# Kernel optimization log

Hardware: AMD Instinct MI355X
Metric: run time of the kernel (lower is better)

## Reference

```python
import jax, jax.numpy as jnp
import numpy as np

EPS = 1e-09

def setup_inputs() -> dict:
    key = jax.random.key(0)
    k1, k2, k3 = jax.random.split(key, 3)
    B, C, H, W = 16, 512, 64, 64
    K = 64  # node_num
    x = jax.random.normal(k1, (B, C, H, W), dtype=jnp.float32)
    anchor = jax.random.uniform(k2, (K, C), dtype=jnp.float32)
    sigma_raw = jax.random.uniform(k3, (K, C), dtype=jnp.float32)
    return {"x": x, "anchor": anchor, "sigma_raw": sigma_raw}

def _l2norm(v, axis):
    return v / jnp.maximum(jnp.linalg.norm(v, axis=axis, keepdims=True), 1e-12)

def reference(x, anchor, sigma_raw):
    B, C, H, W = x.shape
    K = anchor.shape[0]
    N = H * W
    sigma = jax.nn.sigmoid(sigma_raw)               # [K, C]
    xf = x.reshape(B, C, N).transpose(0, 2, 1)      # [B, N, C] descriptors

    # squared Mahalanobis-like distance ||(x - a_k)/s_k||^2 via expansion
    # (avoids materializing the [B, N, K, C] residual the torch loop builds)
    inv_s2 = 1.0 / (sigma * sigma)                  # [K, C]
    a_s2 = anchor * inv_s2                          # [K, C]
    const = jnp.sum(anchor * a_s2, axis=1)          # [K]
    d2 = (jnp.einsum('bnc,kc->bnk', xf * xf, inv_s2)
          - 2.0 * jnp.einsum('bnc,kc->bnk', xf, a_s2)
          + const[None, None, :])                   # [B, N, K]
    logits = (-0.5 * d2).transpose(0, 2, 1)         # [B, K, N]
    soft_assign = jax.nn.softmax(logits, axis=1)    # softmax over nodes

    # aggregation: nodes[b,k,c] = sum_n w * (x - a_k)/s_k / (sum_n w + eps)
    w_sum = jnp.sum(soft_assign, axis=2)            # [B, K]
    wx = jnp.einsum('bkn,bnc->bkc', soft_assign, xf)  # [B, K, C]
    nodes = (wx - w_sum[:, :, None] * anchor[None]) / sigma[None]
    nodes = nodes / (w_sum[:, :, None] + EPS)       # [B, K, C]

    nodes = _l2norm(nodes, axis=2)                  # intra-normalize per node
    flat = _l2norm(nodes.reshape(B, -1), axis=1)    # global L2
    # faithful to torch: flat [B, K*C] reinterpreted (no transpose) as [B, C, K]
    return flat.reshape(B, C, K), soft_assign
```

## Files before the change

### kernel.cpp

```cpp
#include <hip/hip_runtime.h>
#include <math.h>

#define B_ 16
#define C_ 512
#define N_ 4096
#define K_ 64

#define OFF_PBIG    0
#define OFF_INVSIG  131072
#define OFF_WSUM    163840
#define OFF_GSUM    164864
#define OFF_WX      164992

typedef short bf16x8 __attribute__((ext_vector_type(8)));
typedef float f32x16 __attribute__((ext_vector_type(16)));

union U4 { uint4 u; bf16x8 b; };

__device__ __forceinline__ unsigned hi16(float f) { return __float_as_uint(f) >> 16; }
__device__ __forceinline__ unsigned hi16rne(float f) {
  return (__float_as_uint(f) + 0x8000u) >> 16;
}
__device__ __forceinline__ float fromhi(unsigned h) { return __uint_as_float(h << 16); }
__device__ __forceinline__ unsigned pk(float lo, float hi) {
  return (__float_as_uint(lo) >> 16) | (__float_as_uint(hi) & 0xFFFF0000u);
}

__global__ void k_prep(const float* __restrict__ anchor,
                       const float* __restrict__ sraw,
                       unsigned* __restrict__ pbig,
                       float* __restrict__ invsig,
                       float* __restrict__ wsum,
                       float* __restrict__ gsum) {
  const int k = blockIdx.x;
  const int t = threadIdx.x;
  __shared__ float s_is2[C_], s_m[C_];
  __shared__ float red[4];
  float part = 0.f;
#pragma unroll
  for (int r = 0; r < 2; r++) {
    int c = r * 256 + t;
    float a = anchor[k * C_ + c];
    float sg = 1.f / (1.f + __expf(-sraw[k * C_ + c]));
    float is = 1.f / sg;
    float is2 = is * is;
    s_is2[c] = is2;
    s_m[c] = -2.f * a * is2;
    invsig[k * C_ + c] = is;
    part = fmaf(a * a, is2, part);
  }
  float v = part;
#pragma unroll
  for (int off = 32; off; off >>= 1) v += __shfl_down(v, off);
  if ((t & 63) == 0) red[t >> 6] = v;
  __syncthreads();
  float cst = red[0] + red[1] + red[2] + red[3];
  unsigned ch = hi16(cst);
  unsigned clr = hi16rne(cst - fromhi(ch));
#pragma unroll
  for (int r = 0; r < 2; r++) {
    int c = r * 256 + t;
    float is2 = s_is2[c], m = s_m[c];
    unsigned ih = hi16(is2);
    unsigned ilr = hi16rne(is2 - fromhi(ih));
    unsigned mh = hi16(m);
    unsigned mlr = hi16rne(m - fromhi(mh));
    unsigned* p = pbig + (size_t)k * 2048 + c * 4;
    p[0] = ih | (ilr << 16);
    p[1] = ih | (mh << 16);
    p[2] = mlr | (mh << 16);
    p[3] = (c == 0) ? (ch | (clr << 16)) : 0u;
  }
  if (k == 0) {
    for (int i = t; i < B_ * K_; i += 256) wsum[i] = 0.f;
    if (t < B_) gsum[t] = 0.f;
  }
}

__global__ __launch_bounds__(256) void k_dist(
    const float* __restrict__ x,
    const unsigned* __restrict__ pbig,
    float* __restrict__ soft,
    float* __restrict__ wsum) {
  const int b = blockIdx.y;
  const int nblk = blockIdx.x * 256;
  const int tid = threadIdx.x;
  const int wid = tid >> 6;
  const int lane = tid & 63;
  const int l31 = lane & 31;
  const int lh = lane >> 5;
  const int n0 = nblk + wid * 64;

  __shared__ unsigned ldsA[64 * 132];

  f32x16 acc[2][2];
#pragma unroll
  for (int kt = 0; kt < 2; kt++)
#pragma unroll
    for (int ns = 0; ns < 2; ns++)
#pragma unroll
      for (int i = 0; i < 16; i++) acc[kt][ns][i] = 0.f;

  const float* xb = x + (size_t)b * (C_ * N_);

  for (int chunk = 0; chunk < 16; chunk++) {
    const uint4* src = (const uint4*)pbig;
#pragma unroll
    for (int it = 0; it < 8; it++) {
      int flat = tid + it * 256;
      int k = flat >> 5, q = flat & 31;
      uint4 vv = src[(size_t)k * 512 + chunk * 32 + q];
      *(uint4*)&ldsA[k * 132 + q * 4] = vv;
    }
    __syncthreads();
    const int cchunk = chunk * 32;
    for (int kstep = 0; kstep < 16; kstep++) {
      U4 a0, a1;
      a0.u = *(const uint4*)&ldsA[l31 * 132 + kstep * 8 + lh * 4];
      a1.u = *(const uint4*)&ldsA[(32 + l31) * 132 + kstep * 8 + lh * 4];
      const int c = cchunk + kstep * 2 + lh;
      const float* xr = xb + (size_t)c * N_;
#pragma unroll
      for (int ns = 0; ns < 2; ns++) {
        float xv = xr[n0 + ns * 32 + l31];
        float x2 = xv * xv;
        unsigned u = __float_as_uint(xv);
        unsigned u2 = __float_as_uint(x2);
        unsigned uhf = u & 0xFFFF0000u;
        unsigned u2hf = u2 & 0xFFFF0000u;
        float xl = xv - __uint_as_float(uhf);
        float x2l = x2 - __uint_as_float(u2hf);
        U4 bf;
        bf.u.x = (u2 >> 16) | u2hf;
        bf.u.y = ((__float_as_uint(x2l) + 0x8000u) >> 16) | uhf;
        bf.u.z = (u >> 16) | ((__float_as_uint(xl) + 0x8000u) & 0xFFFF0000u);
        bf.u.w = (c == 0) ? 0x3F803F80u : 0u;
        acc[0][ns] = __builtin_amdgcn_mfma_f32_32x32x16_bf16(a0.b, bf.b, acc[0][ns], 0, 0, 0);
        acc[1][ns] = __builtin_amdgcn_mfma_f32_32x32x16_bf16(a1.b, bf.b, acc[1][ns], 0, 0, 0);
      }
    }
    __syncthreads();
  }

  float* softb = soft + (size_t)b * (K_ * N_);
#pragma unroll
  for (int ns = 0; ns < 2; ns++) {
    float mm = -3.4e38f;
#pragma unroll
    for (int kt = 0; kt < 2; kt++)
#pragma unroll
      for (int r = 0; r < 16; r++) {
        float l = -0.5f * acc[kt][ns][r];
        acc[kt][ns][r] = l;
        mm = fmaxf(mm, l);
      }
    mm = fmaxf(mm, __shfl_xor(mm, 32));
    float ss = 0.f;
#pragma unroll
    for (int kt = 0; kt < 2; kt++)
#pragma unroll
      for (int r = 0; r < 16; r++) {
        float e = __expf(acc[kt][ns][r] - mm);
        acc[kt][ns][r] = e;
        ss += e;
      }
    ss += __shfl_xor(ss, 32);
    float inv = 1.f / ss;
    const int nc = n0 + ns * 32 + l31;
#pragma unroll
    for (int kt = 0; kt < 2; kt++)
#pragma unroll
      for (int r = 0; r < 16; r++) {
        float w = acc[kt][ns][r] * inv;
        acc[kt][ns][r] = w;
        int k = kt * 32 + (r & 3) + 8 * (r >> 2) + 4 * lh;
        softb[(size_t)k * N_ + nc] = w;
      }
  }
#pragma unroll
  for (int kt = 0; kt < 2; kt++)
#pragma unroll
    for (int r = 0; r < 16; r++) {
      float v = acc[kt][0][r] + acc[kt][1][r];
      v += __shfl_xor(v, 1);
      v += __shfl_xor(v, 2);
      v += __shfl_xor(v, 4);
      v += __shfl_xor(v, 8);
      v += __shfl_xor(v, 16);
      if (l31 == 0) {
        int k = kt * 32 + (r & 3) + 8 * (r >> 2) + 4 * lh;
        atomicAdd(&wsum[b * K_ + k], v);
      }
    }
}

__global__ __launch_bounds__(256) void k_agg(const float* __restrict__ x,
                                             const float* __restrict__ soft,
                                             float* __restrict__ wx) {
  const int ct = blockIdx.x;
  const int b = blockIdx.y;
  const int tid = threadIdx.x;
  const int wid = tid >> 6, lane = tid & 63, l31 = lane & 31, lh = lane >> 5;
  const int c0 = ct * 32;
  const int n0 = wid * 1024;
  __shared__ float red[4][64][36];

  f32x16 acc[2];
#pragma unroll
  for (int kt = 0; kt < 2; kt++)
#pragma unroll
    for (int i = 0; i < 16; i++) acc[kt][i] = 0.f;

  const float* sb = soft + (size_t)b * (K_ * N_);
  const float* xr = x + (size_t)b * (C_ * N_) + (size_t)(c0 + l31) * N_;
  const float* s0 = sb + (size_t)l31 * N_;
  const float* s1 = sb + (size_t)(32 + l31) * N_;

  for (int kstep = 0; kstep < 64; kstep++) {
    int nb = n0 + kstep * 16 + lh * 8;
    float4 f0 = *(const float4*)&s0[nb];
    float4 f1 = *(const float4*)&s0[nb + 4];
    float4 g0 = *(const float4*)&s1[nb];
    float4 g1 = *(const float4*)&s1[nb + 4];
    float4 h0 = *(const float4*)&xr[nb];
    float4 h1 = *(const float4*)&xr[nb + 4];
    U4 A0, A1, Bf;
    A0.u.x = pk(f0.x, f0.y); A0.u.y = pk(f0.z, f0.w);
    A0.u.z = pk(f1.x, f1.y); A0.u.w = pk(f1.z, f1.w);
    A1.u.x = pk(g0.x, g0.y); A1.u.y = pk(g0.z, g0.w);
    A1.u.z = pk(g1.x, g1.y); A1.u.w = pk(g1.z, g1.w);
    Bf.u.x = pk(h0.x, h0.y); Bf.u.y = pk(h0.z, h0.w);
    Bf.u.z = pk(h1.x, h1.y); Bf.u.w = pk(h1.z, h1.w);
    acc[0] = __builtin_amdgcn_mfma_f32_32x32x16_bf16(A0.b, Bf.b, acc[0], 0, 0, 0);
    acc[1] = __builtin_amdgcn_mfma_f32_32x32x16_bf16(A1.b, Bf.b, acc[1], 0, 0, 0);
  }
#pragma unroll
  for (int kt = 0; kt < 2; kt++)
#pragma unroll
    for (int q = 0; q < 4; q++) {
      float4 vv = make_float4(acc[kt][q * 4], acc[kt][q * 4 + 1],
                              acc[kt][q * 4 + 2], acc[kt][q * 4 + 3]);
      *(float4*)&red[wid][lane][kt * 16 + q * 4] = vv;
    }
  __syncthreads();
  const int lt = tid & 63, sb4 = (tid >> 6) * 8;
  float v[8];
#pragma unroll
  for (int i = 0; i < 8; i++) v[i] = 0.f;
#pragma unroll
  for (int w = 0; w < 4; w++)
#pragma unroll
    for (int i = 0; i < 8; i++) v[i] += red[w][lt][sb4 + i];
#pragma unroll
  for (int i = 0; i < 8; i++) {
    int s = sb4 + i;
    int kt = s >> 4, r = s & 15;
    int k = kt * 32 + (r & 3) + 8 * (r >> 2) + 4 * (lt >> 5);
    wx[((size_t)b * K_ + k) * C_ + c0 + (lt & 31)] = v[i];
  }
}

__global__ void k_nodes(const float* __restrict__ wx,
                        const float* __restrict__ wsum,
                        const float* __restrict__ anchor,
                        const float* __restrict__ invsig,
                        float* __restrict__ out0,
                        float* __restrict__ gsum) {
  const int k = blockIdx.x, b = blockIdx.y;
  const int tid = threadIdx.x;
  float wsv = wsum[b * K_ + k];
  float winv = 1.f / (wsv + 1e-9f);
  float vals[4];
  float local = 0.f;
#pragma unroll
  for (int r = 0; r < 4; r++) {
    int c = r * 128 + tid;
    float w = wx[((size_t)b * K_ + k) * C_ + c];
    float v = (w - wsv * anchor[k * C_ + c]) * invsig[k * C_ + c] * winv;
    vals[r] = v;
    local = fmaf(v, v, local);
  }
  float v = local;
#pragma unroll
  for (int off = 32; off; off >>= 1) v += __shfl_down(v, off);
  __shared__ float red[2];
  if ((tid & 63) == 0) red[tid >> 6] = v;
  __syncthreads();
  float sumsq = red[0] + red[1];
  float norm = sqrtf(sumsq);
  float scale = 1.f / fmaxf(norm, 1e-12f);
#pragma unroll
  for (int r = 0; r < 4; r++) {
    int c = r * 128 + tid;
    out0[((size_t)b * K_ + k) * C_ + c] = vals[r] * scale;
  }
  if (tid == 0) atomicAdd(&gsum[b], sumsq * scale * scale);
}

__global__ void k_final(float* __restrict__ out0,
                        const float* __restrict__ gsum) {
  for (int i = blockIdx.x * 256 + threadIdx.x; i < B_ * K_ * C_;
       i += gridDim.x * 256) {
    int b = i >> 15;
    out0[i] = out0[i] * (1.f / fmaxf(sqrtf(gsum[b]), 1e-12f));
  }
}

extern "C" void kernel_launch(void* const* d_in, const int* in_sizes, int n_in,
                              void* d_out, int out_size, void* d_ws, size_t ws_size,
                              hipStream_t stream) {
  const float* x = (const float*)d_in[0];
  const float* anchor = (const float*)d_in[1];
  const float* sraw = (const float*)d_in[2];
  float* out0 = (float*)d_out;
  float* soft = out0 + (size_t)B_ * C_ * K_;
  float* ws = (float*)d_ws;

  unsigned* pbig = (unsigned*)(ws + OFF_PBIG);
  float* invsig = ws + OFF_INVSIG;
  float* wsum = ws + OFF_WSUM;
  float* gsum = ws + OFF_GSUM;
  float* wx = ws + OFF_WX;

  k_prep<<<K_, 256, 0, stream>>>(anchor, sraw, pbig, invsig, wsum, gsum);
  k_dist<<<dim3(N_ / 256, B_), 256, 0, stream>>>(x, pbig, soft, wsum);
  k_agg<<<dim3(C_ / 32, B_), 256, 0, stream>>>(x, soft, wx);
  k_nodes<<<dim3(K_, B_), 128, 0, stream>>>(wx, wsum, anchor, invsig, out0,
                                            gsum);
  k_final<<<512, 256, 0, stream>>>(out0, gsum);
}
```

Before: 305.6 us.

## Prefetch operands, split aggregation over N with LDS tiling, hoist per-node constant

The distance kernel now stages the next chunk's parameters and x values in registers while the current chunk runs on MFMA. Each wave handles 32 positions instead of 64 and the grid is doubled. The per-node constant is added after the matmul instead of being folded into a bf16 slot. The aggregation kernel is restructured to split N into four partitions, tile soft-assign and x through LDS with register prefetch, and write partial sums that the node kernel adds up. Rounding of the low bf16 halves changes from round-to-nearest to truncation, which slightly alters accuracy, and the partial-sum buffer adds extra workspace traffic.

```diff
diff --git a/kernel.cpp b/kernel.cpp
--- a/kernel.cpp
+++ b/kernel.cpp
@@ -7,10 +7,11 @@
 #define K_ 64
 
 #define OFF_PBIG    0
-#define OFF_INVSIG  131072
-#define OFF_WSUM    163840
-#define OFF_GSUM    164864
-#define OFF_WX      164992
+#define OFF_CONST   131072
+#define OFF_INVSIG  131136
+#define OFF_WSUM    163904
+#define OFF_GSUM    164928
+#define OFF_WXP     165120
 
 typedef short bf16x8 __attribute__((ext_vector_type(8)));
 typedef float f32x16 __attribute__((ext_vector_type(16)));
@@ -18,9 +19,6 @@
 union U4 { uint4 u; bf16x8 b; };
 
 __device__ __forceinline__ unsigned hi16(float f) { return __float_as_uint(f) >> 16; }
-__device__ __forceinline__ unsigned hi16rne(float f) {
-  return (__float_as_uint(f) + 0x8000u) >> 16;
-}
 __device__ __forceinline__ float fromhi(unsigned h) { return __uint_as_float(h << 16); }
 __device__ __forceinline__ unsigned pk(float lo, float hi) {
   return (__float_as_uint(lo) >> 16) | (__float_as_uint(hi) & 0xFFFF0000u);
@@ -29,6 +27,7 @@
 __global__ void k_prep(const float* __restrict__ anchor,
                        const float* __restrict__ sraw,
                        unsigned* __restrict__ pbig,
+                       float* __restrict__ constk,
                        float* __restrict__ invsig,
                        float* __restrict__ wsum,
                        float* __restrict__ gsum) {
@@ -54,22 +53,20 @@
   for (int off = 32; off; off >>= 1) v += __shfl_down(v, off);
   if ((t & 63) == 0) red[t >> 6] = v;
   __syncthreads();
-  float cst = red[0] + red[1] + red[2] + red[3];
-  unsigned ch = hi16(cst);
-  unsigned clr = hi16rne(cst - fromhi(ch));
+  if (t == 0) constk[k] = red[0] + red[1] + red[2] + red[3];
 #pragma unroll
   for (int r = 0; r < 2; r++) {
     int c = r * 256 + t;
     float is2 = s_is2[c], m = s_m[c];
     unsigned ih = hi16(is2);
-    unsigned ilr = hi16rne(is2 - fromhi(ih));
+    unsigned il = hi16(is2 - fromhi(ih));
     unsigned mh = hi16(m);
-    unsigned mlr = hi16rne(m - fromhi(mh));
+    unsigned ml = hi16(m - fromhi(mh));
     unsigned* p = pbig + (size_t)k * 2048 + c * 4;
-    p[0] = ih | (ilr << 16);
+    p[0] = ih | (il << 16);
     p[1] = ih | (mh << 16);
-    p[2] = mlr | (mh << 16);
-    p[3] = (c == 0) ? (ch | (clr << 16)) : 0u;
+    p[2] = ml | (mh << 16);
+    p[3] = 0u;
   }
   if (k == 0) {
     for (int i = t; i < B_ * K_; i += 256) wsum[i] = 0.f;
@@ -80,108 +77,118 @@
 __global__ __launch_bounds__(256) void k_dist(
     const float* __restrict__ x,
     const unsigned* __restrict__ pbig,
+    const float* __restrict__ constk,
     float* __restrict__ soft,
     float* __restrict__ wsum) {
   const int b = blockIdx.y;
-  const int nblk = blockIdx.x * 256;
   const int tid = threadIdx.x;
-  const int wid = tid >> 6;
-  const int lane = tid & 63;
-  const int l31 = lane & 31;
-  const int lh = lane >> 5;
-  const int n0 = nblk + wid * 64;
-
+  const int wid = tid >> 6, lane = tid & 63, l31 = lane & 31, lh = lane >> 5;
+  const int n0 = blockIdx.x * 128 + wid * 32;
   __shared__ unsigned ldsA[64 * 132];
-
-  f32x16 acc[2][2];
-#pragma unroll
-  for (int kt = 0; kt < 2; kt++)
-#pragma unroll
-    for (int ns = 0; ns < 2; ns++)
-#pragma unroll
-      for (int i = 0; i < 16; i++) acc[kt][ns][i] = 0.f;
+  __shared__ float csh[64];
+  if (tid < 64) csh[tid] = constk[tid];
+
+  f32x16 acc[2];
+#pragma unroll
+  for (int kt = 0; kt < 2; kt++)
+#pragma unroll
+    for (int i = 0; i < 16; i++) acc[kt][i] = 0.f;
 
   const float* xb = x + (size_t)b * (C_ * N_);
+  const uint4* src = (const uint4*)pbig;
+
+  uint4 preg[8];
+#pragma unroll
+  for (int it = 0; it < 8; it++) {
+    int flat = tid + it * 256;
+    preg[it] = src[(size_t)(flat >> 5) * 512 + (flat & 31)];
+  }
+  float xcur[16], xnext[16];
+#pragma unroll
+  for (int i = 0; i < 16; i++)
+    xcur[i] = xb[(size_t)(i * 2 + lh) * N_ + n0 + l31];
 
   for (int chunk = 0; chunk < 16; chunk++) {
-    const uint4* src = (const uint4*)pbig;
 #pragma unroll
     for (int it = 0; it < 8; it++) {
       int flat = tid + it * 256;
-      int k = flat >> 5, q = flat & 31;
-      uint4 vv = src[(size_t)k * 512 + chunk * 32 + q];
-      *(uint4*)&ldsA[k * 132 + q * 4] = vv;
+      *(uint4*)&ldsA[(flat >> 5) * 132 + (flat & 31) * 4] = preg[it];
     }
     __syncthreads();
-    const int cchunk = chunk * 32;
+    if (chunk < 15) {
+#pragma unroll
+      for (int it = 0; it < 8; it++) {
+        int flat = tid + it * 256;
+        preg[it] = src[(size_t)(flat >> 5) * 512 + (chunk + 1) * 32 + (flat & 31)];
+      }
+#pragma unroll
+      for (int i = 0; i < 16; i++)
+        xnext[i] = xb[(size_t)((chunk + 1) * 32 + i * 2 + lh) * N_ + n0 + l31];
+    }
+#pragma unroll
     for (int kstep = 0; kstep < 16; kstep++) {
       U4 a0, a1;
       a0.u = *(const uint4*)&ldsA[l31 * 132 + kstep * 8 + lh * 4];
       a1.u = *(const uint4*)&ldsA[(32 + l31) * 132 + kstep * 8 + lh * 4];
-      const int c = cchunk + kstep * 2 + lh;
-      const float* xr = xb + (size_t)c * N_;
-#pragma unroll
-      for (int ns = 0; ns < 2; ns++) {
-        float xv = xr[n0 + ns * 32 + l31];
-        float x2 = xv * xv;
-        unsigned u = __float_as_uint(xv);
-        unsigned u2 = __float_as_uint(x2);
-        unsigned uhf = u & 0xFFFF0000u;
-        unsigned u2hf = u2 & 0xFFFF0000u;
-        float xl = xv - __uint_as_float(uhf);
-        float x2l = x2 - __uint_as_float(u2hf);
-        U4 bf;
-        bf.u.x = (u2 >> 16) | u2hf;
-        bf.u.y = ((__float_as_uint(x2l) + 0x8000u) >> 16) | uhf;
-        bf.u.z = (u >> 16) | ((__float_as_uint(xl) + 0x8000u) & 0xFFFF0000u);
-        bf.u.w = (c == 0) ? 0x3F803F80u : 0u;
-        acc[0][ns] = __builtin_amdgcn_mfma_f32_32x32x16_bf16(a0.b, bf.b, acc[0][ns], 0, 0, 0);
-        acc[1][ns] = __builtin_amdgcn_mfma_f32_32x32x16_bf16(a1.b, bf.b, acc[1][ns], 0, 0, 0);
-      }
+      float xv = xcur[kstep];
+      float x2 = xv * xv;
+      unsigned u = __float_as_uint(xv);
+      unsigned u2 = __float_as_uint(x2);
+      unsigned uhf = u & 0xFFFF0000u;
+      unsigned u2hf = u2 & 0xFFFF0000u;
+      float xl = xv - __uint_as_float(uhf);
+      float x2l = x2 - __uint_as_float(u2hf);
+      U4 bf;
+      bf.u.x = (u2 >> 16) | u2hf;
+      bf.u.y = (__float_as_uint(x2l) >> 16) | uhf;
+      bf.u.z = (u >> 16) | (__float_as_uint(xl) & 0xFFFF0000u);
+      bf.u.w = 0u;
+      acc[0] = __builtin_amdgcn_mfma_f32_32x32x16_bf16(a0.b, bf.b, acc[0], 0, 0, 0);
+      acc[1] = __builtin_amdgcn_mfma_f32_32x32x16_bf16(a1.b, bf.b, acc[1], 0, 0, 0);
     }
     __syncthreads();
-  }
+#pragma unroll
+    for (int i = 0; i < 16; i++) xcur[i] = xnext[i];
+  }
+
+  float mm = -3.4e38f;
+#pragma unroll
+  for (int kt = 0; kt < 2; kt++)
+#pragma unroll
+    for (int r = 0; r < 16; r++) {
+      int k = kt * 32 + (r & 3) + 8 * (r >> 2) + 4 * lh;
+      float l = -0.5f * (acc[kt][r] + csh[k]);
+      acc[kt][r] = l;
+      mm = fmaxf(mm, l);
+    }
+  mm = fmaxf(mm, __shfl_xor(mm, 32));
+  float ss = 0.f;
+#pragma unroll
+  for (int kt = 0; kt < 2; kt++)
+#pragma unroll
+    for (int r = 0; r < 16; r++) {
+      float e = __expf(acc[kt][r] - mm);
+      acc[kt][r] = e;
+      ss += e;
+    }
+  ss += __shfl_xor(ss, 32);
+  float inv = 1.f / ss;
 
   float* softb = soft + (size_t)b * (K_ * N_);
 #pragma unroll
-  for (int ns = 0; ns < 2; ns++) {
-    float mm = -3.4e38f;
-#pragma unroll
-    for (int kt = 0; kt < 2; kt++)
-#pragma unroll
-      for (int r = 0; r < 16; r++) {
-        float l = -0.5f * acc[kt][ns][r];
-        acc[kt][ns][r] = l;
-        mm = fmaxf(mm, l);
-      }
-    mm = fmaxf(mm, __shfl_xor(mm, 32));
-    float ss = 0.f;
-#pragma unroll
-    for (int kt = 0; kt < 2; kt++)
-#pragma unroll
-      for (int r = 0; r < 16; r++) {
-        float e = __expf(acc[kt][ns][r] - mm);
-        acc[kt][ns][r] = e;
-        ss += e;
-      }
-    ss += __shfl_xor(ss, 32);
-    float inv = 1.f / ss;
-    const int nc = n0 + ns * 32 + l31;
-#pragma unroll
-    for (int kt = 0; kt < 2; kt++)
-#pragma unroll
-      for (int r = 0; r < 16; r++) {
-        float w = acc[kt][ns][r] * inv;
-        acc[kt][ns][r] = w;
-        int k = kt * 32 + (r & 3) + 8 * (r >> 2) + 4 * lh;
-        softb[(size_t)k * N_ + nc] = w;
-      }
-  }
-#pragma unroll
-  for (int kt = 0; kt < 2; kt++)
-#pragma unroll
-    for (int r = 0; r < 16; r++) {
-      float v = acc[kt][0][r] + acc[kt][1][r];
+  for (int kt = 0; kt < 2; kt++)
+#pragma unroll
+    for (int r = 0; r < 16; r++) {
+      float w = acc[kt][r] * inv;
+      acc[kt][r] = w;
+      int k = kt * 32 + (r & 3) + 8 * (r >> 2) + 4 * lh;
+      softb[(size_t)k * N_ + n0 + l31] = w;
+    }
+#pragma unroll
+  for (int kt = 0; kt < 2; kt++)
+#pragma unroll
+    for (int r = 0; r < 16; r++) {
+      float v = acc[kt][r];
       v += __shfl_xor(v, 1);
       v += __shfl_xor(v, 2);
       v += __shfl_xor(v, 4);
@@ -196,14 +203,14 @@
 
 __global__ __launch_bounds__(256) void k_agg(const float* __restrict__ x,
                                              const float* __restrict__ soft,
-                                             float* __restrict__ wx) {
+                                             float* __restrict__ wxp) {
   const int ct = blockIdx.x;
-  const int b = blockIdx.y;
+  const int nt = blockIdx.y;
+  const int b = blockIdx.z;
   const int tid = threadIdx.x;
   const int wid = tid >> 6, lane = tid & 63, l31 = lane & 31, lh = lane >> 5;
-  const int c0 = ct * 32;
-  const int n0 = wid * 1024;
-  __shared__ float red[4][64][36];
+  __shared__ unsigned sA[64 * 36];
+  __shared__ unsigned sX[128 * 36];
 
   f32x16 acc[2];
 #pragma unroll
@@ -211,56 +218,68 @@
 #pragma unroll
     for (int i = 0; i < 16; i++) acc[kt][i] = 0.f;
 
-  const float* sb = soft + (size_t)b * (K_ * N_);
-  const float* xr = x + (size_t)b * (C_ * N_) + (size_t)(c0 + l31) * N_;
-  const float* s0 = sb + (size_t)l31 * N_;
-  const float* s1 = sb + (size_t)(32 + l31) * N_;
-
-  for (int kstep = 0; kstep < 64; kstep++) {
-    int nb = n0 + kstep * 16 + lh * 8;
-    float4 f0 = *(const float4*)&s0[nb];
-    float4 f1 = *(const float4*)&s0[nb + 4];
-    float4 g0 = *(const float4*)&s1[nb];
-    float4 g1 = *(const float4*)&s1[nb + 4];
-    float4 h0 = *(const float4*)&xr[nb];
-    float4 h1 = *(const float4*)&xr[nb + 4];
-    U4 A0, A1, Bf;
-    A0.u.x = pk(f0.x, f0.y); A0.u.y = pk(f0.z, f0.w);
-    A0.u.z = pk(f1.x, f1.y); A0.u.w = pk(f1.z, f1.w);
-    A1.u.x = pk(g0.x, g0.y); A1.u.y = pk(g0.z, g0.w);
-    A1.u.z = pk(g1.x, g1.y); A1.u.w = pk(g1.z, g1.w);
-    Bf.u.x = pk(h0.x, h0.y); Bf.u.y = pk(h0.z, h0.w);
-    Bf.u.z = pk(h1.x, h1.y); Bf.u.w = pk(h1.z, h1.w);
-    acc[0] = __builtin_amdgcn_mfma_f32_32x32x16_bf16(A0.b, Bf.b, acc[0], 0, 0, 0);
-    acc[1] = __builtin_amdgcn_mfma_f32_32x32x16_bf16(A1.b, Bf.b, acc[1], 0, 0, 0);
-  }
-#pragma unroll
-  for (int kt = 0; kt < 2; kt++)
-#pragma unroll
-    for (int q = 0; q < 4; q++) {
-      float4 vv = make_float4(acc[kt][q * 4], acc[kt][q * 4 + 1],
-                              acc[kt][q * 4 + 2], acc[kt][q * 4 + 3]);
-      *(float4*)&red[wid][lane][kt * 16 + q * 4] = vv;
-    }
-  __syncthreads();
-  const int lt = tid & 63, sb4 = (tid >> 6) * 8;
-  float v[8];
-#pragma unroll
-  for (int i = 0; i < 8; i++) v[i] = 0.f;
-#pragma unroll
-  for (int w = 0; w < 4; w++)
-#pragma unroll
-    for (int i = 0; i < 8; i++) v[i] += red[w][lt][sb4 + i];
-#pragma unroll
-  for (int i = 0; i < 8; i++) {
-    int s = sb4 + i;
-    int kt = s >> 4, r = s & 15;
-    int k = kt * 32 + (r & 3) + 8 * (r >> 2) + 4 * (lt >> 5);
-    wx[((size_t)b * K_ + k) * C_ + c0 + (lt & 31)] = v[i];
-  }
-}
-
-__global__ void k_nodes(const float* __restrict__ wx,
+  const float* sb = soft + (size_t)b * (K_ * N_) + nt * 1024;
+  const float* xg = x + ((size_t)b * C_ + ct * 128) * N_ + nt * 1024;
+  const int srow = tid >> 2, scol = (tid & 3) * 16;
+  const int xrow = tid >> 1, xcol = (tid & 1) * 32;
+
+  float4 sreg[4], xreg[8];
+#pragma unroll
+  for (int q = 0; q < 4; q++)
+    sreg[q] = *(const float4*)&sb[(size_t)srow * N_ + scol + q * 4];
+#pragma unroll
+  for (int q = 0; q < 8; q++)
+    xreg[q] = *(const float4*)&xg[(size_t)xrow * N_ + xcol + q * 4];
+
+  for (int ch = 0; ch < 16; ch++) {
+    {
+      uint4 w0 = make_uint4(pk(sreg[0].x, sreg[0].y), pk(sreg[0].z, sreg[0].w),
+                            pk(sreg[1].x, sreg[1].y), pk(sreg[1].z, sreg[1].w));
+      uint4 w1 = make_uint4(pk(sreg[2].x, sreg[2].y), pk(sreg[2].z, sreg[2].w),
+                            pk(sreg[3].x, sreg[3].y), pk(sreg[3].z, sreg[3].w));
+      *(uint4*)&sA[srow * 36 + (tid & 3) * 8] = w0;
+      *(uint4*)&sA[srow * 36 + (tid & 3) * 8 + 4] = w1;
+#pragma unroll
+      for (int h = 0; h < 4; h++) {
+        uint4 v = make_uint4(
+            pk(xreg[h * 2].x, xreg[h * 2].y), pk(xreg[h * 2].z, xreg[h * 2].w),
+            pk(xreg[h * 2 + 1].x, xreg[h * 2 + 1].y),
+            pk(xreg[h * 2 + 1].z, xreg[h * 2 + 1].w));
+        *(uint4*)&sX[xrow * 36 + (tid & 1) * 16 + h * 4] = v;
+      }
+    }
+    __syncthreads();
+    if (ch < 15) {
+      int base = (ch + 1) * 64;
+#pragma unroll
+      for (int q = 0; q < 4; q++)
+        sreg[q] = *(const float4*)&sb[(size_t)srow * N_ + base + scol + q * 4];
+#pragma unroll
+      for (int q = 0; q < 8; q++)
+        xreg[q] = *(const float4*)&xg[(size_t)xrow * N_ + base + xcol + q * 4];
+    }
+#pragma unroll
+    for (int kk = 0; kk < 4; kk++) {
+      U4 a0, a1, bf;
+      a0.u = *(const uint4*)&sA[l31 * 36 + kk * 8 + lh * 4];
+      a1.u = *(const uint4*)&sA[(32 + l31) * 36 + kk * 8 + lh * 4];
+      bf.u = *(const uint4*)&sX[(wid * 32 + l31) * 36 + kk * 8 + lh * 4];
+      acc[0] = __builtin_amdgcn_mfma_f32_32x32x16_bf16(a0.b, bf.b, acc[0], 0, 0, 0);
+      acc[1] = __builtin_amdgcn_mfma_f32_32x32x16_bf16(a1.b, bf.b, acc[1], 0, 0, 0);
+    }
+    __syncthreads();
+  }
+  float* outp = wxp + (((size_t)nt * B_ + b) * K_) * C_ + ct * 128 + wid * 32 + l31;
+#pragma unroll
+  for (int kt = 0; kt < 2; kt++)
+#pragma unroll
+    for (int r = 0; r < 16; r++) {
+      int k = kt * 32 + (r & 3) + 8 * (r >> 2) + 4 * lh;
+      outp[(size_t)k * C_] = acc[kt][r];
+    }
+}
+
+__global__ void k_nodes(const float* __restrict__ wxp,
                         const float* __restrict__ wsum,
                         const float* __restrict__ anchor,
                         const float* __restrict__ invsig,
@@ -275,7 +294,10 @@
 #pragma unroll
   for (int r = 0; r < 4; r++) {
     int c = r * 128 + tid;
-    float w = wx[((size_t)b * K_ + k) * C_ + c];
+    float w = 0.f;
+#pragma unroll
+    for (int p = 0; p < 4; p++)
+      w += wxp[(((size_t)p * B_ + b) * K_ + k) * C_ + c];
     float v = (w - wsv * anchor[k * C_ + c]) * invsig[k * C_ + c] * winv;
     vals[r] = v;
     local = fmaf(v, v, local);
@@ -317,15 +339,16 @@
   float* ws = (float*)d_ws;
 
   unsigned* pbig = (unsigned*)(ws + OFF_PBIG);
+  float* constk = ws + OFF_CONST;
   float* invsig = ws + OFF_INVSIG;
   float* wsum = ws + OFF_WSUM;
   float* gsum = ws + OFF_GSUM;
-  float* wx = ws + OFF_WX;
-
-  k_prep<<<K_, 256, 0, stream>>>(anchor, sraw, pbig, invsig, wsum, gsum);
-  k_dist<<<dim3(N_ / 256, B_), 256, 0, stream>>>(x, pbig, soft, wsum);
-  k_agg<<<dim3(C_ / 32, B_), 256, 0, stream>>>(x, soft, wx);
-  k_nodes<<<dim3(K_, B_), 128, 0, stream>>>(wx, wsum, anchor, invsig, out0,
+  float* wxp = ws + OFF_WXP;
+
+  k_prep<<<K_, 256, 0, stream>>>(anchor, sraw, pbig, constk, invsig, wsum, gsum);
+  k_dist<<<dim3(N_ / 128, B_), 256, 0, stream>>>(x, pbig, constk, soft, wsum);
+  k_agg<<<dim3(C_ / 128, 4, B_), 256, 0, stream>>>(x, soft, wxp);
+  k_nodes<<<dim3(K_, B_), 128, 0, stream>>>(wxp, wsum, anchor, invsig, out0,
                                             gsum);
   k_final<<<512, 256, 0, stream>>>(out0, gsum);
 }
```

Result: slower. 362.0 us (+18.5%).
